# Kernel optimization log

Measured on AMD Instinct MI355X. Metric: run time of the kernel, lower is better.

## Reference

```python
import jax, jax.numpy as jnp
import numpy as np
import math

D_MODEL = 1024
D_STATE = 64
D_CONV = 4
HEADDIM = 64
EXPAND = 2
NGROUPS = 1
D_INNER = EXPAND * D_MODEL            # 2048
NHEADS = D_INNER // HEADDIM           # 32
CONV_DIM = D_INNER + 2 * NGROUPS * D_STATE   # 2176
D_IN_PROJ = 2 * D_INNER + 2 * NGROUPS * D_STATE + NHEADS  # 4256
BATCH, SEQLEN = 2, 1024
RMS_EPS = 1.1920929e-07  # torch.finfo(float32).eps (nn.RMSNorm default)


def setup_inputs() -> dict:
    key = jax.random.key(0)
    ks = jax.random.split(key, 8)
    x = jax.random.normal(ks[0], (BATCH, SEQLEN, D_MODEL), dtype=jnp.float32)
    W_in = jax.random.normal(ks[1], (D_IN_PROJ, D_MODEL), dtype=jnp.float32) / math.sqrt(D_MODEL)
    conv_w = jax.random.normal(ks[2], (CONV_DIM, D_CONV), dtype=jnp.float32) / math.sqrt(D_CONV)
    conv_b = jnp.zeros((CONV_DIM,), dtype=jnp.float32)
    # dt_bias init as in the module: inverse-softplus of log-uniform dt
    dt_min, dt_max = 1e-3, 1e-1
    dt = jnp.exp(jax.random.uniform(ks[3], (NHEADS,)) * (math.log(dt_max) - math.log(dt_min)) + math.log(dt_min))
    dt = jnp.clip(dt, 1e-4, None)
    dt_bias = dt + jnp.log(-jnp.expm1(-dt))
    A_log = jnp.log(jax.random.uniform(ks[4], (NHEADS,), minval=1.0, maxval=16.0))
    D_param = jnp.ones((NHEADS,), dtype=jnp.float32)
    norm_w = jnp.ones((D_INNER,), dtype=jnp.float32)
    W_out = jax.random.normal(ks[5], (D_MODEL, D_INNER), dtype=jnp.float32) / math.sqrt(D_INNER)
    return {"x": x, "W_in": W_in, "conv_w": conv_w, "conv_b": conv_b,
            "dt_bias": dt_bias, "A_log": A_log, "D_param": D_param,
            "norm_w": norm_w, "W_out": W_out}


def reference(x, W_in, conv_w, conv_b, dt_bias, A_log, D_param, norm_w, W_out):
    B, L, _ = x.shape
    # input projection: z | xBC | dt_raw
    zxbcdt = x @ W_in.T                                   # (B, L, D_IN_PROJ)
    z = zxbcdt[..., :D_INNER]
    xBC = zxbcdt[..., D_INNER:D_INNER + CONV_DIM]
    dt_raw = zxbcdt[..., D_INNER + CONV_DIM:]
    dt = jax.nn.softplus(dt_raw + dt_bias)                # (B, L, H)

    # depthwise causal conv (left-pad d_conv-1, keep first L outputs)
    xpad = jnp.pad(xBC, ((0, 0), (D_CONV - 1, 0), (0, 0)))
    conv_out = conv_b
    for k in range(D_CONV):  # tiny fixed kernel width
        conv_out = conv_out + xpad[:, k:k + L, :] * conv_w[:, k]
    xBC_conv = jax.nn.silu(conv_out)                      # (B, L, CONV_DIM)

    x_ssm = xBC_conv[..., :D_INNER]
    B_ssm = xBC_conv[..., D_INNER:D_INNER + NGROUPS * D_STATE]
    C_ssm = xBC_conv[..., D_INNER + NGROUPS * D_STATE:]

    x_heads = x_ssm.reshape(B, L, NHEADS, HEADDIM)        # (B, L, H, P)
    hpg = NHEADS // NGROUPS
    B_h = jnp.repeat(B_ssm.reshape(B, L, NGROUPS, D_STATE), hpg, axis=2)  # (B, L, H, N)
    C_h = jnp.repeat(C_ssm.reshape(B, L, NGROUPS, D_STATE), hpg, axis=2)

    A = -jnp.exp(A_log)                                   # (H,)
    dA = jnp.exp(dt * A)                                  # (B, L, H)

    # selective SSM scan: h_t = dA_t * h_{t-1} + dt_t * x_t (outer) B_t ; y_t = h_t . C_t
    def step(h, inp):
        dA_t, dt_t, x_t, B_t, C_t = inp   # (B,H), (B,H), (B,H,P), (B,H,N), (B,H,N)
        h = h * dA_t[:, :, None, None] + (dt_t[:, :, None] * x_t)[..., None] * B_t[:, :, None, :]
        y = jnp.einsum('bhpn,bhn->bhp', h, C_t)
        return h, y

    h0 = jnp.zeros((B, NHEADS, HEADDIM, D_STATE), x.dtype)
    xs = (dA.swapaxes(0, 1), dt.swapaxes(0, 1), x_heads.swapaxes(0, 1),
          B_h.swapaxes(0, 1), C_h.swapaxes(0, 1))
    _, ys = jax.lax.scan(step, h0, xs)                    # ys: (L, B, H, P)
    y_heads = ys.swapaxes(0, 1) + D_param[None, None, :, None] * x_heads

    y = y_heads.reshape(B, L, D_INNER)
    # RMSNorm then SiLU(z) gate
    var = jnp.mean(y * y, axis=-1, keepdims=True)
    y = y * jax.lax.rsqrt(var + RMS_EPS) * norm_w
    y = y * jax.nn.silu(z)
    return y @ W_out.T                                    # (B, L, D_MODEL)
```

## Files before the change

### kernel.cpp

```cpp
#include <hip/hip_runtime.h>
#include <hip/hip_bf16.h>
#include <math.h>

#define D_MODEL   1024
#define D_INNER   2048
#define NHEADS    32
#define HEADDIM   64
#define D_STATE   64
#define CONV_DIM  2176
#define D_IN_PROJ 4256
#define ZXLD      4352
#define BATCH     2
#define SEQLEN    1024
#define BL        (BATCH * SEQLEN)
#define RMS_EPS   1.1920929e-07f

#define QCHUNK 64
#define NC     (SEQLEN / QCHUNK)

typedef __attribute__((ext_vector_type(8))) short short8;
typedef __attribute__((ext_vector_type(4))) float f32x4;
typedef __attribute__((ext_vector_type(8))) unsigned short ushort8v;
typedef __attribute__((ext_vector_type(4))) unsigned short ushort4v;

__device__ __forceinline__ unsigned short f2bf(float f) {
    unsigned u = __builtin_bit_cast(unsigned, f);
    unsigned r = u + 0x7FFFu + ((u >> 16) & 1u);
    return (unsigned short)(r >> 16);
}
__device__ __forceinline__ float bf2f(unsigned short u) {
    unsigned v = ((unsigned)u) << 16;
    return __builtin_bit_cast(float, v);
}
__device__ __forceinline__ void gload_lds16(const void* g, void* l) {
    __builtin_amdgcn_global_load_lds(
        (const __attribute__((address_space(1))) void*)g,
        (__attribute__((address_space(3))) void*)l, 16, 0, 0);
}

#define MFMA_BF16 __builtin_amdgcn_mfma_f32_16x16x32_bf16

template<int BM, int BN, int WR, int WC, bool OBF16>
__global__ __launch_bounds__(256) void gemm_bf16_nt(
    const unsigned short* __restrict__ A, const unsigned short* __restrict__ B,
    void* __restrict__ Cv, int K, int ldc, int nbx)
{
    constexpr int RM = BM / WR;
    constexpr int RN = BN / WC;
    constexpr int MF = RM / 16;
    constexpr int NF = RN / 16;
    constexpr int GA = BM / 32;
    constexpr int GB = BN / 32;

    __shared__ unsigned short As[BM][64];
    __shared__ unsigned short Bs[BN][64];

    const int tid  = threadIdx.x;
    const int lane = tid & 63;
    const int w    = tid >> 6;
    const int wm   = w / WC;
    const int wn   = w % WC;

    const int nwg  = nbx * gridDim.y;
    const int cpx  = nwg >> 3;
    const int orig = blockIdx.y * nbx + blockIdx.x;
    const int swz  = (orig & 7) * cpx + (orig >> 3);
    const int bx   = swz % nbx;
    const int by   = swz / nbx;
    const int m0   = by * BM;
    const int n0   = bx * BN;

    const int srow  = lane >> 3;
    const int sslot = (lane & 7) ^ srow;

    const int fr  = lane & 15;
    const int hq  = lane >> 4;
    const int fr7 = fr & 7;

    f32x4 acc[MF][NF];
#pragma unroll
    for (int mi = 0; mi < MF; ++mi)
#pragma unroll
        for (int ni = 0; ni < NF; ++ni) acc[mi][ni] = (f32x4){0.f, 0.f, 0.f, 0.f};

    for (int k0 = 0; k0 < K; k0 += 64) {
        __syncthreads();
#pragma unroll
        for (int q = 0; q < GA; ++q) {
            const int g8 = (w * GA + q) * 8;
            gload_lds16(A + (size_t)(m0 + g8 + srow) * K + k0 + sslot * 8,
                        &As[g8][0]);
        }
#pragma unroll
        for (int q = 0; q < GB; ++q) {
            const int g8 = (w * GB + q) * 8;
            gload_lds16(B + (size_t)(n0 + g8 + srow) * K + k0 + sslot * 8,
                        &Bs[g8][0]);
        }
        __syncthreads();

#pragma unroll
        for (int ks = 0; ks < 2; ++ks) {
            const int slot = (ks * 4 + hq) ^ fr7;
            short8 av[MF], bv[NF];
#pragma unroll
            for (int mi = 0; mi < MF; ++mi)
                av[mi] = *(const short8*)&As[wm * RM + mi * 16 + fr][slot * 8];
#pragma unroll
            for (int ni = 0; ni < NF; ++ni)
                bv[ni] = *(const short8*)&Bs[wn * RN + ni * 16 + fr][slot * 8];
#pragma unroll
            for (int mi = 0; mi < MF; ++mi)
#pragma unroll
                for (int ni = 0; ni < NF; ++ni)
                    acc[mi][ni] = MFMA_BF16(av[mi], bv[ni], acc[mi][ni], 0, 0, 0);
        }
    }

    const int crow = (lane >> 4) * 4;
    const int ccol = lane & 15;
#pragma unroll
    for (int mi = 0; mi < MF; ++mi)
#pragma unroll
        for (int ni = 0; ni < NF; ++ni) {
            const int row0 = m0 + wm * RM + mi * 16 + crow;
            const int col  = n0 + wn * RN + ni * 16 + ccol;
#pragma unroll
            for (int r = 0; r < 4; ++r) {
                if constexpr (OBF16) {
                    ((unsigned short*)Cv)[(size_t)(row0 + r) * ldc + col] =
                        f2bf(acc[mi][ni][r]);
                } else {
                    ((float*)Cv)[(size_t)(row0 + r) * ldc + col] = acc[mi][ni][r];
                }
            }
        }
}

#define CAST_N1 (BL * D_MODEL / 4)
#define CAST_N2 (ZXLD * D_MODEL / 4)
#define CAST_N3 (D_MODEL * D_INNER / 4)

__global__ __launch_bounds__(256) void cast_all_kernel(
    const float* __restrict__ x, const float* __restrict__ W_in,
    const float* __restrict__ W_out,
    unsigned short* __restrict__ xb, unsigned short* __restrict__ winb,
    unsigned short* __restrict__ woutb)
{
    const int i = blockIdx.x * 256 + threadIdx.x;
    if (i < CAST_N1) {
        float4 v = *(const float4*)(x + (size_t)i * 4);
        ushort4 o = {f2bf(v.x), f2bf(v.y), f2bf(v.z), f2bf(v.w)};
        *(ushort4*)(xb + (size_t)i * 4) = o;
    } else if (i < CAST_N1 + CAST_N2) {
        const int j = i - CAST_N1;
        const int e0 = j * 4;
        const int row = e0 >> 10;
        ushort4 o = {0, 0, 0, 0};
        if (row < D_IN_PROJ) {
            float4 v = *(const float4*)(W_in + (size_t)e0);
            o.x = f2bf(v.x); o.y = f2bf(v.y); o.z = f2bf(v.z); o.w = f2bf(v.w);
        }
        *(ushort4*)(winb + (size_t)e0) = o;
    } else if (i < CAST_N1 + CAST_N2 + CAST_N3) {
        const int j = i - CAST_N1 - CAST_N2;
        float4 v = *(const float4*)(W_out + (size_t)j * 4);
        ushort4 o = {f2bf(v.x), f2bf(v.y), f2bf(v.z), f2bf(v.w)};
        *(ushort4*)(woutb + (size_t)j * 4) = o;
    }
}

__global__ __launch_bounds__(256) void conv_pre_kernel(
    const unsigned short* __restrict__ zxb,
    const float* __restrict__ conv_w, const float* __restrict__ conv_b,
    const float* __restrict__ dt_bias,
    unsigned short* __restrict__ xTb, unsigned short* __restrict__ Bcc,
    unsigned short* __restrict__ BTc, unsigned short* __restrict__ Ccc,
    float* __restrict__ dtt)
{
    const int c = blockIdx.x;
    const int g = blockIdx.y;
    const int b = blockIdx.z;
    const int tid = threadIdx.x;

    const int l0 = c * QCHUNK;
    const int grow0 = b * SEQLEN + l0;

    if (g == 17) {
        const int hd = tid & 31;
        const int t0 = (tid >> 5) * 8;
        const float bias = dt_bias[hd];
#pragma unroll
        for (int j = 0; j < 8; ++j) {
            const int row = t0 + j;
            const float v = bf2f(zxb[(size_t)(grow0 + row) * ZXLD +
                                     (D_INNER + CONV_DIM) + hd]) + bias;
            const float sp = (v > 20.f) ? v : log1pf(__expf(v));
            dtt[((size_t)b * NHEADS + hd) * SEQLEN + l0 + row] = sp;
        }
        return;
    }

    __shared__ unsigned short L[64][138];
    const int r = tid >> 2;
    const int q = (tid & 3) * 16;

    for (int hh = 0; hh < 2; ++hh) {
        const int chbase = g * 128 + hh * 64;
        float in[4][16];
#pragma unroll
        for (int k = 0; k < 4; ++k) {
            const int ll = l0 + r - 3 + k;
            if (ll >= 0) {
                const unsigned short* src =
                    zxb + (size_t)(grow0 + r - 3 + k) * ZXLD + (D_INNER + chbase + q);
                ushort8v v0 = *(const ushort8v*)(src);
                ushort8v v1 = *(const ushort8v*)(src + 8);
#pragma unroll
                for (int j = 0; j < 8; ++j) { in[k][j] = bf2f(v0[j]); in[k][8 + j] = bf2f(v1[j]); }
            } else {
#pragma unroll
                for (int j = 0; j < 16; ++j) in[k][j] = 0.f;
            }
        }
        unsigned short o[16];
#pragma unroll
        for (int j = 0; j < 16; ++j) {
            const int ch = chbase + q + j;
            const float4 wv = *(const float4*)(conv_w + ch * 4);
            float a = conv_b[ch];
            a = fmaf(in[0][j], wv.x, a);
            a = fmaf(in[1][j], wv.y, a);
            a = fmaf(in[2][j], wv.z, a);
            a = fmaf(in[3][j], wv.w, a);
            o[j] = f2bf(a / (1.f + __expf(-a)));
        }

        const bool isB = (g == 16) && (hh == 0);
        const bool isC = (g == 16) && (hh == 1);
        const size_t ctile = ((size_t)b * NC + c) * 4096;

        if (isB || isC) {
            unsigned short* dst = (isB ? Bcc : Ccc) + ctile + (size_t)r * 64 + q;
            ushort8v w0, w1;
#pragma unroll
            for (int j = 0; j < 8; ++j) { w0[j] = o[j]; w1[j] = o[8 + j]; }
            *(ushort8v*)dst = w0;
            *(ushort8v*)(dst + 8) = w1;
        }
        if (!isC) {
#pragma unroll
            for (int j = 0; j < 8; ++j) { L[r][q + j] = o[j]; L[r][q + 8 + j] = o[8 + j]; }
            __syncthreads();
            const int cc = tid >> 2;
            const int tseg = (tid & 3) * 16;
            unsigned short tv[16];
#pragma unroll
            for (int j = 0; j < 16; ++j) tv[j] = L[tseg + j][cc];
            unsigned short* dstT;
            if (isB) dstT = BTc + ctile + (size_t)cc * 64 + tseg;
            else {
                const int hgt = g * 2 + hh;
                dstT = xTb + (((size_t)b * NHEADS + hgt) * NC + c) * 4096 + (size_t)cc * 64 + tseg;
            }
            ushort8v w0, w1;
#pragma unroll
            for (int j = 0; j < 8; ++j) { w0[j] = tv[j]; w1[j] = tv[8 + j]; }
            *(ushort8v*)dstT = w0;
            *(ushort8v*)(dstT + 8) = w1;
        }
        __syncthreads();
    }
}

__global__ __launch_bounds__(256) void chunk_state_kernel(
    const unsigned short* __restrict__ xTb, const unsigned short* __restrict__ BTc,
    const float* __restrict__ dtt, const float* __restrict__ A_log,
    unsigned short* __restrict__ Sintra, float* __restrict__ cumA)
{
    const int bid = blockIdx.x;
    const int c = bid & (NC - 1);
    const int h = (bid >> 4) & (NHEADS - 1);
    const int b = bid >> 9;
    const int tid = threadIdx.x;
    const int lane = tid & 63;
    const int w = tid >> 6;

    __shared__ unsigned short sXT[64][72];
    __shared__ unsigned short sBT[64][72];
    __shared__ float sw[64];

    if (tid < QCHUNK) {
        const float A = -__expf(A_log[h]);
        const float dtv = dtt[((size_t)b * NHEADS + h) * SEQLEN + c * QCHUNK + tid];
        float cum = dtv * A;
#pragma unroll
        for (int off = 1; off < 64; off <<= 1) {
            const float o = __shfl_up(cum, off, 64);
            if (tid >= off) cum += o;
        }
        const float cum_end = __shfl(cum, 63, 64);
        sw[tid] = __expf(cum_end - cum) * dtv;
        cumA[(size_t)bid * QCHUNK + tid] = cum;
    }
    __syncthreads();

    {
        const int r = tid >> 2, q = (tid & 3) * 16;
        const unsigned short* xs =
            xTb + (((size_t)b * NHEADS + h) * NC + c) * 4096 + (size_t)r * 64 + q;
        ushort8v v0 = *(const ushort8v*)(xs);
        ushort8v v1 = *(const ushort8v*)(xs + 8);
        ushort8v s0, s1;
#pragma unroll
        for (int j = 0; j < 8; ++j) {
            s0[j] = f2bf(bf2f(v0[j]) * sw[q + j]);
            s1[j] = f2bf(bf2f(v1[j]) * sw[q + 8 + j]);
        }
        *(ushort8v*)&sXT[r][q] = s0;
        *(ushort8v*)&sXT[r][q + 8] = s1;

        const unsigned short* bs =
            BTc + ((size_t)b * NC + c) * 4096 + (size_t)r * 64 + q;
        *(ushort8v*)&sBT[r][q]     = *(const ushort8v*)(bs);
        *(ushort8v*)&sBT[r][q + 8] = *(const ushort8v*)(bs + 8);
    }
    __syncthreads();

    const int fr = lane & 15;
    const int ko = (lane >> 4) * 8;
    short8 a0 = *(const short8*)&sBT[w * 16 + fr][ko];
    short8 a1 = *(const short8*)&sBT[w * 16 + fr][ko + 32];

    unsigned short* sout = Sintra + (size_t)bid * (D_STATE * HEADDIM);
    const int nrow = w * 16 + (lane >> 4) * 4;
#pragma unroll
    for (int j = 0; j < 4; ++j) {
        short8 b0 = *(const short8*)&sXT[j * 16 + fr][ko];
        short8 b1 = *(const short8*)&sXT[j * 16 + fr][ko + 32];
        f32x4 a = (f32x4){0.f, 0.f, 0.f, 0.f};
        a = MFMA_BF16(a0, b0, a, 0, 0, 0);
        a = MFMA_BF16(a1, b1, a, 0, 0, 0);
        const int p = j * 16 + fr;
#pragma unroll
        for (int r = 0; r < 4; ++r)
            sout[(size_t)(nrow + r) * HEADDIM + p] = f2bf(a[r]);
    }
}

__global__ __launch_bounds__(256) void state_pass_kernel(
    unsigned short* __restrict__ S, const float* __restrict__ cumA)
{
    const int gid = blockIdx.x * 256 + threadIdx.x;
    const int bh = gid >> 10;
    const int e0 = (gid & 1023) * 4;

    float run[4] = {0.f, 0.f, 0.f, 0.f};
    unsigned short* base = S + (size_t)bh * NC * (D_STATE * HEADDIM) + e0;

    ushort4v pre = *(const ushort4v*)base;
    float gpre = __expf(cumA[((size_t)bh * NC) * QCHUNK + (QCHUNK - 1)]);

    for (int c = 0; c < NC; ++c) {
        const ushort4v cur = pre;
        const float g = gpre;
        if (c + 1 < NC) {
            pre = *(const ushort4v*)(base + (size_t)(c + 1) * (D_STATE * HEADDIM));
            gpre = __expf(cumA[((size_t)bh * NC + c + 1) * QCHUNK + (QCHUNK - 1)]);
        }
        ushort4v o;
#pragma unroll
        for (int j = 0; j < 4; ++j) o[j] = f2bf(run[j]);
        *(ushort4v*)(base + (size_t)c * (D_STATE * HEADDIM)) = o;
#pragma unroll
        for (int j = 0; j < 4; ++j) run[j] = fmaf(g, run[j], bf2f(cur[j]));
    }
}

__global__ __launch_bounds__(256) void chunk_output_kernel(
    const unsigned short* __restrict__ xTb, const unsigned short* __restrict__ Bcc,
    const unsigned short* __restrict__ Ccc, const float* __restrict__ dtt,
    const unsigned short* __restrict__ SP, const float* __restrict__ cumA,
    const float* __restrict__ D_param, unsigned short* __restrict__ y)
{
    const int bid = blockIdx.x;
    const int c = bid & (NC - 1);
    const int h = (bid >> 4) & (NHEADS - 1);
    const int b = bid >> 9;
    const int tid = threadIdx.x;
    const int lane = tid & 63;
    const int w = tid >> 6;

    __shared__ unsigned short sC[64][72];
    __shared__ unsigned short sB[64][72];
    __shared__ unsigned short sXT[64][72];
    __shared__ unsigned short sSPT[64][72];
    __shared__ unsigned short sM[64][72];
    __shared__ float scum[64], sdt[64];

    const size_t ctile = ((size_t)b * NC + c) * 4096;
    {
        const int r = tid >> 2, q = (tid & 3) * 16;
        const unsigned short* cs = Ccc + ctile + (size_t)r * 64 + q;
        *(ushort8v*)&sC[r][q]     = *(const ushort8v*)(cs);
        *(ushort8v*)&sC[r][q + 8] = *(const ushort8v*)(cs + 8);
        const unsigned short* bs = Bcc + ctile + (size_t)r * 64 + q;
        *(ushort8v*)&sB[r][q]     = *(const ushort8v*)(bs);
        *(ushort8v*)&sB[r][q + 8] = *(const ushort8v*)(bs + 8);
        const unsigned short* xs =
            xTb + (((size_t)b * NHEADS + h) * NC + c) * 4096 + (size_t)r * 64 + q;
        *(ushort8v*)&sXT[r][q]     = *(const ushort8v*)(xs);
        *(ushort8v*)&sXT[r][q + 8] = *(const ushort8v*)(xs + 8);
        const unsigned short* ss = SP + (size_t)bid * (D_STATE * HEADDIM) + (size_t)r * 64 + q;
        ushort8v v0 = *(const ushort8v*)(ss);
        ushort8v v1 = *(const ushort8v*)(ss + 8);
#pragma unroll
        for (int j = 0; j < 8; ++j) { sSPT[q + j][r] = v0[j]; sSPT[q + 8 + j][r] = v1[j]; }
    }
    if (tid < QCHUNK) {
        scum[tid] = cumA[(size_t)bid * QCHUNK + tid];
        sdt[tid] = dtt[((size_t)b * NHEADS + h) * SEQLEN + c * QCHUNK + tid];
    }
    __syncthreads();

    const int fr = lane & 15;
    const int ko = (lane >> 4) * 8;
    const int trow = w * 16 + (lane >> 4) * 4;

    short8 aC0 = *(const short8*)&sC[w * 16 + fr][ko];
    short8 aC1 = *(const short8*)&sC[w * 16 + fr][ko + 32];

    f32x4 g[4];
#pragma unroll
    for (int j = 0; j < 4; ++j) {
        short8 b0 = *(const short8*)&sB[j * 16 + fr][ko];
        short8 b1 = *(const short8*)&sB[j * 16 + fr][ko + 32];
        f32x4 a = (f32x4){0.f, 0.f, 0.f, 0.f};
        a = MFMA_BF16(aC0, b0, a, 0, 0, 0);
        a = MFMA_BF16(aC1, b1, a, 0, 0, 0);
        g[j] = a;
    }

    float ct[4];
#pragma unroll
    for (int r = 0; r < 4; ++r) ct[r] = scum[trow + r];
#pragma unroll
    for (int j = 0; j < 4; ++j) {
        const int s = j * 16 + fr;
        const float cs = scum[s], ds = sdt[s];
#pragma unroll
        for (int r = 0; r < 4; ++r) {
            const int t = trow + r;
            const float m = (s <= t) ? g[j][r] * __expf(ct[r] - cs) * ds : 0.f;
            sM[t][s] = f2bf(m);
        }
    }
    __syncthreads();

    short8 aM0 = *(const short8*)&sM[w * 16 + fr][ko];
    short8 aM1 = *(const short8*)&sM[w * 16 + fr][ko + 32];
    f32x4 y1[4], y2[4];
#pragma unroll
    for (int j = 0; j < 4; ++j) {
        short8 bx0 = *(const short8*)&sXT[j * 16 + fr][ko];
        short8 bx1 = *(const short8*)&sXT[j * 16 + fr][ko + 32];
        f32x4 a = (f32x4){0.f, 0.f, 0.f, 0.f};
        a = MFMA_BF16(aM0, bx0, a, 0, 0, 0);
        a = MFMA_BF16(aM1, bx1, a, 0, 0, 0);
        y1[j] = a;
        short8 bs0 = *(const short8*)&sSPT[j * 16 + fr][ko];
        short8 bs1 = *(const short8*)&sSPT[j * 16 + fr][ko + 32];
        f32x4 a2 = (f32x4){0.f, 0.f, 0.f, 0.f};
        a2 = MFMA_BF16(aC0, bs0, a2, 0, 0, 0);
        a2 = MFMA_BF16(aC1, bs1, a2, 0, 0, 0);
        y2[j] = a2;
    }

    const float Dp = D_param[h];
    float et[4];
#pragma unroll
    for (int r = 0; r < 4; ++r) et[r] = __expf(ct[r]);
    unsigned short* ybase = y + (((size_t)b * SEQLEN + c * QCHUNK) * D_INNER) + h * HEADDIM;
#pragma unroll
    for (int j = 0; j < 4; ++j) {
        const int p = j * 16 + fr;
#pragma unroll
        for (int r = 0; r < 4; ++r) {
            const int t = trow + r;
            const float xv = bf2f(sXT[p][t]);
            ybase[(size_t)t * D_INNER + p] = f2bf(y1[j][r] + et[r] * y2[j][r] + Dp * xv);
        }
    }
}

__global__ __launch_bounds__(256) void rms_gate_kernel(
    const unsigned short* __restrict__ y, const unsigned short* __restrict__ zxb,
    const float* __restrict__ norm_w, unsigned short* __restrict__ out)
{
    const int m = blockIdx.x;
    const int tid = threadIdx.x;
    const unsigned short* yr = y + (size_t)m * D_INNER;
    const unsigned short* zr = zxb + (size_t)m * ZXLD;

    ushort8v yv8 = *(const ushort8v*)(yr + tid * 8);
    float yv[8];
#pragma unroll
    for (int j = 0; j < 8; ++j) yv[j] = bf2f(yv8[j]);
    float ss = 0.f;
#pragma unroll
    for (int j = 0; j < 8; ++j) ss += yv[j] * yv[j];
#pragma unroll
    for (int off = 32; off > 0; off >>= 1) ss += __shfl_xor(ss, off, 64);
    __shared__ float sred[4];
    if ((tid & 63) == 0) sred[tid >> 6] = ss;
    __syncthreads();
    const float tot = sred[0] + sred[1] + sred[2] + sred[3];
    const float inv = rsqrtf(tot * (1.f / D_INNER) + RMS_EPS);

    ushort8v zv8 = *(const ushort8v*)(zr + tid * 8);
    const float* nw = norm_w + tid * 8;
    ushort8v o;
#pragma unroll
    for (int j = 0; j < 8; ++j) {
        const float zz = bf2f(zv8[j]);
        const float sig = 1.f / (1.f + __expf(-zz));
        o[j] = f2bf(yv[j] * inv * nw[j] * (zz * sig));
    }
    *(ushort8v*)(out + (size_t)m * D_INNER + tid * 8) = o;
}

extern "C" void kernel_launch(void* const* d_in, const int* in_sizes, int n_in,
                              void* d_out, int out_size, void* d_ws, size_t ws_size,
                              hipStream_t stream)
{
    const float* x       = (const float*)d_in[0];
    const float* W_in    = (const float*)d_in[1];
    const float* conv_w  = (const float*)d_in[2];
    const float* conv_b  = (const float*)d_in[3];
    const float* dt_bias = (const float*)d_in[4];
    const float* A_log   = (const float*)d_in[5];
    const float* D_param = (const float*)d_in[6];
    const float* norm_w  = (const float*)d_in[7];
    const float* W_out   = (const float*)d_in[8];
    float* out = (float*)d_out;

    char* p = (char*)d_ws;
    unsigned short* zxb   = (unsigned short*)p;  p += (size_t)BL * ZXLD * 2;
    float*          dtt   = (float*)p;           p += (size_t)BATCH * NHEADS * SEQLEN * 4;
    float*          cumA  = (float*)p;           p += (size_t)BATCH * NHEADS * SEQLEN * 4;
    unsigned short* Sb    = (unsigned short*)p;  p += (size_t)BATCH * NHEADS * NC * 4096 * 2;
    unsigned short* xTb   = (unsigned short*)p;  p += (size_t)BATCH * NHEADS * NC * 4096 * 2;
    unsigned short* Bcc   = (unsigned short*)p;  p += (size_t)BATCH * NC * 4096 * 2;
    unsigned short* BTc   = (unsigned short*)p;  p += (size_t)BATCH * NC * 4096 * 2;
    unsigned short* Ccc   = (unsigned short*)p;  p += (size_t)BATCH * NC * 4096 * 2;
    unsigned short* ybb   = (unsigned short*)p;  p += (size_t)BL * D_INNER * 2;
    unsigned short* xb    = (unsigned short*)p;  p += (size_t)BL * D_MODEL * 2;
    unsigned short* winb  = (unsigned short*)p;  p += (size_t)ZXLD * D_MODEL * 2;
    unsigned short* woutb = (unsigned short*)p;  p += (size_t)D_MODEL * D_INNER * 2;
    unsigned short* ygb   = (unsigned short*)p;

    cast_all_kernel<<<(CAST_N1 + CAST_N2 + CAST_N3 + 255) / 256, 256, 0, stream>>>(
        x, W_in, W_out, xb, winb, woutb);

    gemm_bf16_nt<128, 128, 2, 2, true><<<dim3(ZXLD / 128, BL / 128), 256, 0, stream>>>(
        xb, winb, zxb, D_MODEL, ZXLD, ZXLD / 128);

    conv_pre_kernel<<<dim3(NC, 18, BATCH), 256, 0, stream>>>(
        zxb, conv_w, conv_b, dt_bias, xTb, Bcc, BTc, Ccc, dtt);
    chunk_state_kernel<<<BATCH * NHEADS * NC, 256, 0, stream>>>(
        xTb, BTc, dtt, A_log, Sb, cumA);
    state_pass_kernel<<<256, 256, 0, stream>>>(Sb, cumA);
    chunk_output_kernel<<<BATCH * NHEADS * NC, 256, 0, stream>>>(
        xTb, Bcc, Ccc, dtt, Sb, cumA, D_param, ybb);
    rms_gate_kernel<<<BL, 256, 0, stream>>>(ybb, zxb, norm_w, ygb);

    gemm_bf16_nt<64, 64, 2, 2, false><<<dim3(D_MODEL / 64, BL / 64), 256, 0, stream>>>(
        ygb, woutb, out, D_INNER, D_MODEL, D_MODEL / 64);
}
```

Before: 106.4 us.

## Fuse conv, dt softplus and chunk-state MFMA into one kernel

Merges the depthwise conv, dt softplus, cumulative-decay scan and intra-chunk state MFMA into one kernel. The x tile now stays in shared memory for the state product instead of going to global and being read back, and the BT buffer plus one launch are removed. In exchange, each non-B/C block recomputes the B-channel convolution locally, and the grid shrinks to fewer, heavier blocks.

New measurement: 108.7 us. +2.2%, slower.

```diff
diff --git a/kernel.cpp b/kernel.cpp
--- a/kernel.cpp
+++ b/kernel.cpp
@@ -170,181 +170,154 @@
     }
 }
 
-__global__ __launch_bounds__(256) void conv_pre_kernel(
+__device__ __forceinline__ void conv_rows16(
+    const unsigned short* __restrict__ zxb, int grow0, int l0, int chbase,
+    const float* __restrict__ conv_w, const float* __restrict__ conv_b,
+    int r, int q, unsigned short o[16])
+{
+    float in[4][16];
+#pragma unroll
+    for (int k = 0; k < 4; ++k) {
+        const int ll = l0 + r - 3 + k;
+        if (ll >= 0) {
+            const unsigned short* src =
+                zxb + (size_t)(grow0 + r - 3 + k) * ZXLD + (D_INNER + chbase + q);
+            ushort8v v0 = *(const ushort8v*)(src);
+            ushort8v v1 = *(const ushort8v*)(src + 8);
+#pragma unroll
+            for (int j = 0; j < 8; ++j) { in[k][j] = bf2f(v0[j]); in[k][8 + j] = bf2f(v1[j]); }
+        } else {
+#pragma unroll
+            for (int j = 0; j < 16; ++j) in[k][j] = 0.f;
+        }
+    }
+#pragma unroll
+    for (int j = 0; j < 16; ++j) {
+        const int ch = chbase + q + j;
+        const float4 wv = *(const float4*)(conv_w + ch * 4);
+        float a = conv_b[ch];
+        a = fmaf(in[0][j], wv.x, a);
+        a = fmaf(in[1][j], wv.y, a);
+        a = fmaf(in[2][j], wv.z, a);
+        a = fmaf(in[3][j], wv.w, a);
+        o[j] = f2bf(a / (1.f + __expf(-a)));
+    }
+}
+
+__global__ __launch_bounds__(256) void conv_scan_kernel(
     const unsigned short* __restrict__ zxb,
     const float* __restrict__ conv_w, const float* __restrict__ conv_b,
-    const float* __restrict__ dt_bias,
+    const float* __restrict__ dt_bias, const float* __restrict__ A_log,
     unsigned short* __restrict__ xTb, unsigned short* __restrict__ Bcc,
-    unsigned short* __restrict__ BTc, unsigned short* __restrict__ Ccc,
-    float* __restrict__ dtt)
+    unsigned short* __restrict__ Ccc, unsigned short* __restrict__ Sb,
+    float* __restrict__ cumA, float* __restrict__ dtt)
 {
     const int c = blockIdx.x;
     const int g = blockIdx.y;
     const int b = blockIdx.z;
     const int tid = threadIdx.x;
+    const int lane = tid & 63;
+    const int w = tid >> 6;
 
     const int l0 = c * QCHUNK;
     const int grow0 = b * SEQLEN + l0;
-
-    if (g == 17) {
-        const int hd = tid & 31;
-        const int t0 = (tid >> 5) * 8;
-        const float bias = dt_bias[hd];
-#pragma unroll
-        for (int j = 0; j < 8; ++j) {
-            const int row = t0 + j;
-            const float v = bf2f(zxb[(size_t)(grow0 + row) * ZXLD +
-                                     (D_INNER + CONV_DIM) + hd]) + bias;
-            const float sp = (v > 20.f) ? v : log1pf(__expf(v));
-            dtt[((size_t)b * NHEADS + hd) * SEQLEN + l0 + row] = sp;
-        }
-        return;
-    }
-
-    __shared__ unsigned short L[64][138];
     const int r = tid >> 2;
     const int q = (tid & 3) * 16;
-
-    for (int hh = 0; hh < 2; ++hh) {
-        const int chbase = g * 128 + hh * 64;
-        float in[4][16];
-#pragma unroll
-        for (int k = 0; k < 4; ++k) {
-            const int ll = l0 + r - 3 + k;
-            if (ll >= 0) {
-                const unsigned short* src =
-                    zxb + (size_t)(grow0 + r - 3 + k) * ZXLD + (D_INNER + chbase + q);
-                ushort8v v0 = *(const ushort8v*)(src);
-                ushort8v v1 = *(const ushort8v*)(src + 8);
-#pragma unroll
-                for (int j = 0; j < 8; ++j) { in[k][j] = bf2f(v0[j]); in[k][8 + j] = bf2f(v1[j]); }
-            } else {
-#pragma unroll
-                for (int j = 0; j < 16; ++j) in[k][j] = 0.f;
-            }
-        }
-        unsigned short o[16];
-#pragma unroll
-        for (int j = 0; j < 16; ++j) {
-            const int ch = chbase + q + j;
-            const float4 wv = *(const float4*)(conv_w + ch * 4);
-            float a = conv_b[ch];
-            a = fmaf(in[0][j], wv.x, a);
-            a = fmaf(in[1][j], wv.y, a);
-            a = fmaf(in[2][j], wv.z, a);
-            a = fmaf(in[3][j], wv.w, a);
-            o[j] = f2bf(a / (1.f + __expf(-a)));
-        }
-
-        const bool isB = (g == 16) && (hh == 0);
-        const bool isC = (g == 16) && (hh == 1);
+    unsigned short o[16];
+
+    if (g == 16) {
         const size_t ctile = ((size_t)b * NC + c) * 4096;
-
-        if (isB || isC) {
-            unsigned short* dst = (isB ? Bcc : Ccc) + ctile + (size_t)r * 64 + q;
+#pragma unroll
+        for (int hh = 0; hh < 2; ++hh) {
+            conv_rows16(zxb, grow0, l0, 2048 + hh * 64, conv_w, conv_b, r, q, o);
+            unsigned short* dst = (hh == 0 ? Bcc : Ccc) + ctile + (size_t)r * 64 + q;
             ushort8v w0, w1;
 #pragma unroll
             for (int j = 0; j < 8; ++j) { w0[j] = o[j]; w1[j] = o[8 + j]; }
             *(ushort8v*)dst = w0;
             *(ushort8v*)(dst + 8) = w1;
         }
-        if (!isC) {
-#pragma unroll
-            for (int j = 0; j < 8; ++j) { L[r][q + j] = o[j]; L[r][q + 8 + j] = o[8 + j]; }
-            __syncthreads();
-            const int cc = tid >> 2;
-            const int tseg = (tid & 3) * 16;
-            unsigned short tv[16];
-#pragma unroll
-            for (int j = 0; j < 16; ++j) tv[j] = L[tseg + j][cc];
-            unsigned short* dstT;
-            if (isB) dstT = BTc + ctile + (size_t)cc * 64 + tseg;
-            else {
-                const int hgt = g * 2 + hh;
-                dstT = xTb + (((size_t)b * NHEADS + hgt) * NC + c) * 4096 + (size_t)cc * 64 + tseg;
-            }
+        return;
+    }
+
+    __shared__ unsigned short L[64][138];
+    __shared__ unsigned short sBT[64][72];
+    __shared__ unsigned short sXT[64][72];
+    __shared__ float sw[2][64];
+
+    conv_rows16(zxb, grow0, l0, 2048, conv_w, conv_b, r, q, o);
+#pragma unroll
+    for (int j = 0; j < 8; ++j) { L[r][q + j] = o[j]; L[r][q + 8 + j] = o[8 + j]; }
+
+    if (w < 2) {
+        const int h = g * 2 + w;
+        const float A = -__expf(A_log[h]);
+        const float vraw = bf2f(zxb[(size_t)(grow0 + lane) * ZXLD +
+                                    (D_INNER + CONV_DIM) + h]) + dt_bias[h];
+        const float dtv = (vraw > 20.f) ? vraw : log1pf(__expf(vraw));
+        float cum = dtv * A;
+#pragma unroll
+        for (int off = 1; off < 64; off <<= 1) {
+            const float t = __shfl_up(cum, off, 64);
+            if (lane >= off) cum += t;
+        }
+        const float cum_end = __shfl(cum, 63, 64);
+        sw[w][lane] = __expf(cum_end - cum) * dtv;
+        cumA[(((size_t)b * NHEADS + h) * NC + c) * QCHUNK + lane] = cum;
+        dtt[((size_t)b * NHEADS + h) * SEQLEN + l0 + lane] = dtv;
+    }
+    __syncthreads();
+
+    const int cc = tid >> 2;
+    const int tseg = (tid & 3) * 16;
+#pragma unroll
+    for (int j = 0; j < 16; ++j) sBT[cc][tseg + j] = L[tseg + j][cc];
+    __syncthreads();
+
+    const int fr = lane & 15;
+    const int ko = (lane >> 4) * 8;
+    const int nrow = w * 16 + (lane >> 4) * 4;
+
+    for (int hh = 0; hh < 2; ++hh) {
+        const int h = g * 2 + hh;
+        conv_rows16(zxb, grow0, l0, h * 64, conv_w, conv_b, r, q, o);
+#pragma unroll
+        for (int j = 0; j < 8; ++j) { L[r][q + j] = o[j]; L[r][q + 8 + j] = o[8 + j]; }
+        __syncthreads();
+
+        unsigned short tv[16];
+#pragma unroll
+        for (int j = 0; j < 16; ++j) tv[j] = L[tseg + j][cc];
+        {
+            unsigned short* dstT =
+                xTb + (((size_t)b * NHEADS + h) * NC + c) * 4096 + (size_t)cc * 64 + tseg;
             ushort8v w0, w1;
 #pragma unroll
             for (int j = 0; j < 8; ++j) { w0[j] = tv[j]; w1[j] = tv[8 + j]; }
             *(ushort8v*)dstT = w0;
             *(ushort8v*)(dstT + 8) = w1;
         }
+#pragma unroll
+        for (int j = 0; j < 16; ++j)
+            sXT[cc][tseg + j] = f2bf(bf2f(tv[j]) * sw[hh][tseg + j]);
         __syncthreads();
-    }
-}
-
-__global__ __launch_bounds__(256) void chunk_state_kernel(
-    const unsigned short* __restrict__ xTb, const unsigned short* __restrict__ BTc,
-    const float* __restrict__ dtt, const float* __restrict__ A_log,
-    unsigned short* __restrict__ Sintra, float* __restrict__ cumA)
-{
-    const int bid = blockIdx.x;
-    const int c = bid & (NC - 1);
-    const int h = (bid >> 4) & (NHEADS - 1);
-    const int b = bid >> 9;
-    const int tid = threadIdx.x;
-    const int lane = tid & 63;
-    const int w = tid >> 6;
-
-    __shared__ unsigned short sXT[64][72];
-    __shared__ unsigned short sBT[64][72];
-    __shared__ float sw[64];
-
-    if (tid < QCHUNK) {
-        const float A = -__expf(A_log[h]);
-        const float dtv = dtt[((size_t)b * NHEADS + h) * SEQLEN + c * QCHUNK + tid];
-        float cum = dtv * A;
-#pragma unroll
-        for (int off = 1; off < 64; off <<= 1) {
-            const float o = __shfl_up(cum, off, 64);
-            if (tid >= off) cum += o;
-        }
-        const float cum_end = __shfl(cum, 63, 64);
-        sw[tid] = __expf(cum_end - cum) * dtv;
-        cumA[(size_t)bid * QCHUNK + tid] = cum;
-    }
-    __syncthreads();
-
-    {
-        const int r = tid >> 2, q = (tid & 3) * 16;
-        const unsigned short* xs =
-            xTb + (((size_t)b * NHEADS + h) * NC + c) * 4096 + (size_t)r * 64 + q;
-        ushort8v v0 = *(const ushort8v*)(xs);
-        ushort8v v1 = *(const ushort8v*)(xs + 8);
-        ushort8v s0, s1;
-#pragma unroll
-        for (int j = 0; j < 8; ++j) {
-            s0[j] = f2bf(bf2f(v0[j]) * sw[q + j]);
-            s1[j] = f2bf(bf2f(v1[j]) * sw[q + 8 + j]);
-        }
-        *(ushort8v*)&sXT[r][q] = s0;
-        *(ushort8v*)&sXT[r][q + 8] = s1;
-
-        const unsigned short* bs =
-            BTc + ((size_t)b * NC + c) * 4096 + (size_t)r * 64 + q;
-        *(ushort8v*)&sBT[r][q]     = *(const ushort8v*)(bs);
-        *(ushort8v*)&sBT[r][q + 8] = *(const ushort8v*)(bs + 8);
-    }
-    __syncthreads();
-
-    const int fr = lane & 15;
-    const int ko = (lane >> 4) * 8;
-    short8 a0 = *(const short8*)&sBT[w * 16 + fr][ko];
-    short8 a1 = *(const short8*)&sBT[w * 16 + fr][ko + 32];
-
-    unsigned short* sout = Sintra + (size_t)bid * (D_STATE * HEADDIM);
-    const int nrow = w * 16 + (lane >> 4) * 4;
-#pragma unroll
-    for (int j = 0; j < 4; ++j) {
-        short8 b0 = *(const short8*)&sXT[j * 16 + fr][ko];
-        short8 b1 = *(const short8*)&sXT[j * 16 + fr][ko + 32];
-        f32x4 a = (f32x4){0.f, 0.f, 0.f, 0.f};
-        a = MFMA_BF16(a0, b0, a, 0, 0, 0);
-        a = MFMA_BF16(a1, b1, a, 0, 0, 0);
-        const int p = j * 16 + fr;
-#pragma unroll
-        for (int r = 0; r < 4; ++r)
-            sout[(size_t)(nrow + r) * HEADDIM + p] = f2bf(a[r]);
+
+        short8 a0 = *(const short8*)&sBT[w * 16 + fr][ko];
+        short8 a1 = *(const short8*)&sBT[w * 16 + fr][ko + 32];
+        unsigned short* sout = Sb + (((size_t)b * NHEADS + h) * NC + c) * 4096;
+#pragma unroll
+        for (int j = 0; j < 4; ++j) {
+            short8 b0 = *(const short8*)&sXT[j * 16 + fr][ko];
+            short8 b1 = *(const short8*)&sXT[j * 16 + fr][ko + 32];
+            f32x4 a = (f32x4){0.f, 0.f, 0.f, 0.f};
+            a = MFMA_BF16(a0, b0, a, 0, 0, 0);
+            a = MFMA_BF16(a1, b1, a, 0, 0, 0);
+            const int p = j * 16 + fr;
+#pragma unroll
+            for (int rr = 0; rr < 4; ++rr)
+                sout[(size_t)(nrow + rr) * HEADDIM + p] = f2bf(a[rr]);
+        }
+        __syncthreads();
     }
 }
 
@@ -551,7 +524,6 @@
     unsigned short* Sb    = (unsigned short*)p;  p += (size_t)BATCH * NHEADS * NC * 4096 * 2;
     unsigned short* xTb   = (unsigned short*)p;  p += (size_t)BATCH * NHEADS * NC * 4096 * 2;
     unsigned short* Bcc   = (unsigned short*)p;  p += (size_t)BATCH * NC * 4096 * 2;
-    unsigned short* BTc   = (unsigned short*)p;  p += (size_t)BATCH * NC * 4096 * 2;
     unsigned short* Ccc   = (unsigned short*)p;  p += (size_t)BATCH * NC * 4096 * 2;
     unsigned short* ybb   = (unsigned short*)p;  p += (size_t)BL * D_INNER * 2;
     unsigned short* xb    = (unsigned short*)p;  p += (size_t)BL * D_MODEL * 2;
@@ -565,10 +537,8 @@
     gemm_bf16_nt<128, 128, 2, 2, true><<<dim3(ZXLD / 128, BL / 128), 256, 0, stream>>>(
         xb, winb, zxb, D_MODEL, ZXLD, ZXLD / 128);
 
-    conv_pre_kernel<<<dim3(NC, 18, BATCH), 256, 0, stream>>>(
-        zxb, conv_w, conv_b, dt_bias, xTb, Bcc, BTc, Ccc, dtt);
-    chunk_state_kernel<<<BATCH * NHEADS * NC, 256, 0, stream>>>(
-        xTb, BTc, dtt, A_log, Sb, cumA);
+    conv_scan_kernel<<<dim3(NC, 17, BATCH), 256, 0, stream>>>(
+        zxb, conv_w, conv_b, dt_bias, A_log, xTb, Bcc, Ccc, Sb, cumA, dtt);
     state_pass_kernel<<<256, 256, 0, stream>>>(Sb, cumA);
     chunk_output_kernel<<<BATCH * NHEADS * NC, 256, 0, stream>>>(
         xTb, Bcc, Ccc, dtt, Sb, cumA, D_param, ybb);
```
